# Performance work log

Hardware: AMD Instinct MI355X
Metric: run time of the kernel (lower is better)

The kernel has to match this reference:

```python
import jax, jax.numpy as jnp
import numpy as np

S, LC = 8192, 16
CE = CH = 64      # char embed == char hidden (original quirk)
WE, HW = 128, 256 # word embed, word hidden
WV, CV, TAGS = 50000, 128, 50


def _lstm_step(h, c, x, Wih, Whh, bih, bhh):
    # PyTorch LSTM gate order: i, f, g, o
    g = x @ Wih.T + h @ Whh.T + bih + bhh
    i, f, gg, o = jnp.split(g, 4, axis=-1)
    c = jax.nn.sigmoid(f) * c + jax.nn.sigmoid(i) * jnp.tanh(gg)
    h = jax.nn.sigmoid(o) * jnp.tanh(c)
    return h, c


def setup_inputs() -> dict:
    key = jax.random.key(0)
    ks = jax.random.split(key, 16)
    inp = {
        'word_idxs': jax.random.randint(ks[0], (S,), 0, WV),
        'char_idxs': jax.random.randint(ks[1], (S, LC), 0, CV),
        'char_lens': jax.random.randint(ks[2], (S,), 1, LC + 1),
        'char_emb': jax.random.normal(ks[3], (CV, CE), jnp.float32) * 0.1,
        'char_Wih': jax.random.normal(ks[4], (4 * CH, CE), jnp.float32) * 0.1,
        'char_Whh': jax.random.normal(ks[5], (4 * CH, CH), jnp.float32) * 0.1,
        'char_bih': jax.random.normal(ks[6], (4 * CH,), jnp.float32) * 0.1,
        'char_bhh': jax.random.normal(ks[7], (4 * CH,), jnp.float32) * 0.1,
        'word_emb': jax.random.normal(ks[8], (WV, WE), jnp.float32) * 0.1,
        'word_Wih': jax.random.normal(ks[9], (4 * HW, WE + CH), jnp.float32) * 0.1,
        'word_Whh': jax.random.normal(ks[10], (4 * HW, HW), jnp.float32) * 0.1,
        'word_bih': jax.random.normal(ks[11], (4 * HW,), jnp.float32) * 0.1,
        'word_bhh': jax.random.normal(ks[12], (4 * HW,), jnp.float32) * 0.1,
        'tag_W': jax.random.normal(ks[13], (TAGS, HW), jnp.float32) * 0.1,
        'tag_b': jax.random.normal(ks[14], (TAGS,), jnp.float32) * 0.1,
    }
    return inp


def reference(word_idxs, char_idxs, char_lens,
              char_emb, char_Wih, char_Whh, char_bih, char_bhh,
              word_emb, word_Wih, word_Whh, word_bih, word_bhh,
              tag_W, tag_b):
    # --- char LSTM over all words in parallel (one fused scan over char time) ---
    cx = char_emb[char_idxs]                      # [S, LC, CE]
    cx = jnp.transpose(cx, (1, 0, 2))             # [LC, S, CE]

    def cstep(carry, x_t):
        h, c = carry
        h, c = _lstm_step(h, c, x_t, char_Wih, char_Whh, char_bih, char_bhh)
        return (h, c), h

    h0 = jnp.zeros((S, CH), cx.dtype)
    (_, _), hs = jax.lax.scan(cstep, (h0, h0), cx)  # hs: [LC, S, CH]
    # original takes char_lstm_out[-1] == hidden at position len(chars)-1
    char_feat = hs[char_lens - 1, jnp.arange(S)]    # [S, CH]

    # --- word LSTM over the sentence (batch = 1) ---
    wx = jnp.concatenate([word_emb[word_idxs], char_feat], axis=-1)  # [S, WE+CH]

    def wstep(carry, x_t):
        h, c = carry
        h, c = _lstm_step(h, c, x_t, word_Wih, word_Whh, word_bih, word_bhh)
        return (h, c), h

    wh0 = jnp.zeros((HW,), wx.dtype)
    (_, _), outs = jax.lax.scan(wstep, (wh0, wh0), wx)  # [S, HW]

    logits = outs @ tag_W.T + tag_b                     # [S, TAGS]
    return jax.nn.log_softmax(logits, axis=-1)
```

## Files before the change

kernel.cpp:

```cpp
#include <hip/hip_runtime.h>
#include <hip/hip_bf16.h>
#include <hip/hip_fp16.h>

#define S_LEN 8192
#define LC 16
#define CE 64
#define CH 64
#define WE 128
#define NTAGS 50

using bf16 = __hip_bfloat16;
typedef unsigned int u32;
typedef unsigned long long u64;

__device__ __forceinline__ float bfbits2f(unsigned short u) {
    union { unsigned int i; float f; } v; v.i = ((unsigned int)u) << 16; return v.f;
}
__device__ __forceinline__ float sigm(float x) {
    return __builtin_amdgcn_rcpf(1.0f + __expf(-x));
}
__device__ __forceinline__ float tanh_fast(float x) {
    return 1.0f - 2.0f * __builtin_amdgcn_rcpf(__expf(2.0f * x) + 1.0f);
}

template <bool BF>
__device__ __forceinline__ float ld1(const void* p, size_t i) {
    if constexpr (BF) return bfbits2f(((const unsigned short*)p)[i]);
    else              return ((const float*)p)[i];
}
template <bool BF>
__device__ __forceinline__ float4 ld4(const void* p, size_t i) {
    if constexpr (BF) {
        const ushort4 s = *reinterpret_cast<const ushort4*>((const unsigned short*)p + i);
        return make_float4(bfbits2f(s.x), bfbits2f(s.y), bfbits2f(s.z), bfbits2f(s.w));
    } else {
        return *reinterpret_cast<const float4*>((const float*)p + i);
    }
}
template <bool BF>
__device__ __forceinline__ void st1(void* p, size_t i, float v) {
    if constexpr (BF) ((bf16*)p)[i] = __float2bfloat16(v);
    else              ((float*)p)[i] = v;
}

typedef _Float16 h2t __attribute__((ext_vector_type(2)));

__device__ __forceinline__ u32 pk2(float a, float b) {
    __half2 h = __floats2half2_rn(a, b);
    u32 r; __builtin_memcpy(&r, &h, 4); return r;
}
__device__ __forceinline__ float fdot2u(u32 a, u32 b, float c) {
#if __has_builtin(__builtin_amdgcn_fdot2)
    h2t av, bv;
    __builtin_memcpy(&av, &a, 4);
    __builtin_memcpy(&bv, &b, 4);
    return __builtin_amdgcn_fdot2(av, bv, c, false);
#else
    __half2 ah, bh;
    __builtin_memcpy(&ah, &a, 4);
    __builtin_memcpy(&bh, &b, 4);
    c = fmaf(__half2float(ah.x), __half2float(bh.x), c);
    c = fmaf(__half2float(ah.y), __half2float(bh.y), c);
    return c;
#endif
}

__global__ void kdetect(const void* emb, u32* flag, u32* gen) {
    const int j = threadIdx.x;
    int s = 0;
    #pragma unroll
    for (int k = 0; k < 4; ++k) {
        const unsigned short u = ((const unsigned short*)emb)[j * 4 + k];
        const int e = (u >> 7) & 0xFF;
        s += (e >= 100 && e <= 133) ? 1 : 0;
    }
    #pragma unroll
    for (int off = 32; off >= 1; off >>= 1) s += __shfl_xor(s, off, 64);
    if (j == 0) { *flag = (s >= 200) ? 1u : 0u; *gen = *gen + 1u; }
}

template <bool BF>
__global__ __launch_bounds__(256, 2) void kchar(
        const u32* __restrict__ dtf,
        const int* __restrict__ char_idxs, const int* __restrict__ char_lens,
        const void* __restrict__ char_emb,
        const void* __restrict__ Wih, const void* __restrict__ Whh,
        const void* __restrict__ bih, const void* __restrict__ bhh,
        float* __restrict__ cfeat) {
    if ((*dtf != 0u) != BF) return;
    const int j = threadIdx.x;
    const int w0 = blockIdx.x * 8;

    __shared__ __align__(16) float emb_lds[128 * CE];
    __shared__ __align__(16) float gates_lds[8 * 256];
    __shared__ __align__(16) float h_lds[8 * CH];
    __shared__ __align__(16) float c_lds[8 * CH];
    __shared__ int cidx_lds[8 * LC];
    __shared__ int len_lds[8];

    {
        float4* emb4 = reinterpret_cast<float4*>(emb_lds);
        #pragma unroll
        for (int i = 0; i < 8; ++i) {
            const int c = i * 256 + j;
            emb4[c] = ld4<BF>(char_emb, (size_t)c * 4);
        }
    }
    if (j < 128) cidx_lds[j] = char_idxs[w0 * LC + j];
    if (j < 8)   len_lds[j]  = char_lens[w0 + j];
    h_lds[j] = 0.f; h_lds[j + 256] = 0.f;
    c_lds[j] = 0.f; c_lds[j + 256] = 0.f;

    float4 wih4[16], whh4[16];
    #pragma unroll
    for (int kc = 0; kc < 16; ++kc) {
        wih4[kc] = ld4<BF>(Wih, (size_t)j * CE + kc * 4);
        whh4[kc] = ld4<BF>(Whh, (size_t)j * CH + kc * 4);
    }
    const float bias = ld1<BF>(bih, j) + ld1<BF>(bhh, j);
    __syncthreads();

    for (int t = 0; t < LC; ++t) {
        for (int w = 0; w < 8; ++w) {
            const int ci = cidx_lds[w * LC + t];
            const float4* x4  = reinterpret_cast<const float4*>(emb_lds + ci * CE);
            const float4* hh4 = reinterpret_cast<const float4*>(h_lds + w * CH);
            float a0 = 0.f, a1 = 0.f, a2 = 0.f, a3 = 0.f;
            #pragma unroll
            for (int kc = 0; kc < 16; ++kc) {
                const float4 xv = x4[kc]; const float4 hv = hh4[kc];
                const float4 wi = wih4[kc]; const float4 wh = whh4[kc];
                a0 = fmaf(wi.x, xv.x, a0); a1 = fmaf(wi.y, xv.y, a1);
                a2 = fmaf(wi.z, xv.z, a2); a3 = fmaf(wi.w, xv.w, a3);
                a0 = fmaf(wh.x, hv.x, a0); a1 = fmaf(wh.y, hv.y, a1);
                a2 = fmaf(wh.z, hv.z, a2); a3 = fmaf(wh.w, hv.w, a3);
            }
            gates_lds[w * 256 + j] = bias + ((a0 + a1) + (a2 + a3));
        }
        __syncthreads();
        #pragma unroll
        for (int rep = 0; rep < 2; ++rep) {
            const int p = j + rep * 256;
            const int w = p >> 6, u = p & 63;
            const float ig = gates_lds[w * 256 + u];
            const float fg = gates_lds[w * 256 + 64 + u];
            const float gg = gates_lds[w * 256 + 128 + u];
            const float og = gates_lds[w * 256 + 192 + u];
            const float cn = sigm(fg) * c_lds[p] + sigm(ig) * tanh_fast(gg);
            const float hn = sigm(og) * tanh_fast(cn);
            c_lds[p] = cn; h_lds[p] = hn;
            if (t == len_lds[w] - 1)
                cfeat[(size_t)(w0 + w) * CH + u] = hn;
        }
        __syncthreads();
    }
}

template <bool BF>
__global__ __launch_bounds__(256) void kgx(
        const u32* __restrict__ dtf,
        int t0, const int* __restrict__ word_idxs, const float* __restrict__ cfeat,
        const void* __restrict__ wemb, const void* __restrict__ Wih,
        const void* __restrict__ bih, const void* __restrict__ bhh,
        float* __restrict__ Gxr) {
    if ((*dtf != 0u) != BF) return;
    const int j = threadIdx.x;
    const int wr0 = blockIdx.x * 16;
    const int w0g = t0 + wr0;
    __shared__ __align__(16) float wx[16 * 192];
    __shared__ int widx[16];
    if (j < 16) widx[j] = word_idxs[w0g + j];
    __syncthreads();
    {
        const int w = j >> 4, ch = j & 15;
        const size_t eb = (size_t)widx[w] * WE + ch * 8;
        const float4 f0 = ld4<BF>(wemb, eb), f1 = ld4<BF>(wemb, eb + 4);
        float4* dst = reinterpret_cast<float4*>(wx + w * 192 + ch * 8);
        dst[0] = f0; dst[1] = f1;
        const float4 cf = *reinterpret_cast<const float4*>(
            cfeat + (size_t)(w0g + w) * CH + ch * 4);
        *reinterpret_cast<float4*>(wx + w * 192 + WE + ch * 4) = cf;
    }
    __syncthreads();

    for (int g = 0; g < 4; ++g) {
        const int r = g * 256 + j;
        float acc[16];
        #pragma unroll
        for (int w = 0; w < 16; ++w) acc[w] = 0.f;
        #pragma unroll 8
        for (int kc = 0; kc < 48; ++kc) {
            const float4 wv = ld4<BF>(Wih, (size_t)r * 192 + kc * 4);
            #pragma unroll
            for (int w = 0; w < 16; ++w) {
                const float4 xv = *reinterpret_cast<const float4*>(wx + w * 192 + kc * 4);
                acc[w] = fmaf(wv.x, xv.x, acc[w]);
                acc[w] = fmaf(wv.y, xv.y, acc[w]);
                acc[w] = fmaf(wv.z, xv.z, acc[w]);
                acc[w] = fmaf(wv.w, xv.w, acc[w]);
            }
        }
        const float bias = ld1<BF>(bih, r) + ld1<BF>(bhh, r);
        #pragma unroll
        for (int w = 0; w < 16; ++w)
            Gxr[(size_t)(wr0 + w) * 1024 + r] = acc[w] + bias;
    }
}

template <bool BF>
__global__ __launch_bounds__(256, 1) void kwlstm(
        const u32* __restrict__ dtf,
        int t0, int t1, int epoch, const void* __restrict__ whh,
        const float* __restrict__ Gxr,
        float* __restrict__ hallr, u64* hgx2, float* csave, u32* xccpub,
        const u32* __restrict__ genp) {
    if ((*dtf != 0u) != BF) return;
    const int j = threadIdx.x;

    __shared__ int role_s;
    const u32 et = (((*genp) << 8) + (u32)epoch) & 0xFFFFFFu;
    if (j == 0) {
        const u32 xcc = __builtin_amdgcn_s_getreg(6164) & 0xFu;
        __hip_atomic_store(&xccpub[blockIdx.x], (et << 8) | xcc,
                           __ATOMIC_RELAXED, __HIP_MEMORY_SCOPE_AGENT);
    }
    if (j < 64) {
        u32 v;
        do {
            v = __hip_atomic_load(&xccpub[j], __ATOMIC_RELAXED,
                                  __HIP_MEMORY_SCOPE_AGENT);
        } while ((v >> 8) != et);
        const u32 v0 = __shfl(v, 0, 64);
        const u64 mask = __ballot((v & 0xFFu) == (v0 & 0xFFu));
        const int myb = blockIdx.x;
        int role = -1;
        if (__popcll(mask) >= 4) {
            if ((mask >> myb) & 1ull) {
                const int rank = __popcll(mask & ((1ull << myb) - 1ull));
                if (rank < 4) role = rank;
            }
        } else {
            if (myb < 4) role = myb;
        }
        if (j == 0) role_s = role;
    }
    __syncthreads();
    const int b = role_s;
    if (b < 0) return;

    const int w = j >> 6;
    const int l = j & 63;
    const int m = l & 15;
    const int g = l >> 4;
    const int u = w * 16 + m;
    const int R = g * 256 + b * 64 + u;

    __shared__ __align__(16) u32 hsc[4][32];

    u32 wv2[128];
    #pragma unroll
    for (int q = 0; q < 4; ++q) {
        const int qq = (b + q) & 3;
        #pragma unroll
        for (int kc = 0; kc < 8; ++kc) {
            const float4 wa = ld4<BF>(whh, (size_t)R * 256 + qq * 64 + kc * 8);
            const float4 wb = ld4<BF>(whh, (size_t)R * 256 + qq * 64 + kc * 8 + 4);
            wv2[q * 32 + 4 * kc + 0] = pk2(wa.x, wa.y);
            wv2[q * 32 + 4 * kc + 1] = pk2(wa.z, wa.w);
            wv2[q * 32 + 4 * kc + 2] = pk2(wb.x, wb.y);
            wv2[q * 32 + 4 * kc + 3] = pk2(wb.z, wb.w);
        }
    }

    float c_reg = 0.f;
    if (t0 > 0 && l < 16) c_reg = csave[b * 64 + u];

    float gxA = Gxr[(size_t)0 * 1024 + R];
    float gxB = (t0 + 1 < t1) ? Gxr[(size_t)1 * 1024 + R] : 0.f;

    for (int t = t0; t < t1; ++t) {
        const int p = t & 1;
        float gxN = (t + 2 < t1) ? Gxr[(size_t)(t + 2 - t0) * 1024 + R] : 0.f;

        float a0 = 0.f, a1 = 0.f, a2 = 0.f, a3 = 0.f;
        if (t > 0) {
            u32* hsc_w = &hsc[w][0];
            #pragma unroll
            for (int q = 0; q < 4; ++q) {
                const int qq = (b + q) & 3;
                u64* src = &hgx2[(size_t)p * 256 + qq * 64 + l];
                u64 pk;
                for (;;) {
                    pk = __hip_atomic_load(src, __ATOMIC_RELAXED,
                                           __HIP_MEMORY_SCOPE_AGENT);
                    if (__all((u32)(pk >> 32) == (u32)t)) break;
                }
                const float hv = __uint_as_float((u32)pk);
                const float ho = __shfl_xor(hv, 1, 64);
                if (!(l & 1)) hsc_w[l >> 1] = pk2(hv, ho);
                asm volatile("" ::: "memory");
                #pragma unroll
                for (int kc = 0; kc < 8; ++kc) {
                    const u32 hx = hsc_w[4 * kc + 0];
                    const u32 hy = hsc_w[4 * kc + 1];
                    const u32 hz = hsc_w[4 * kc + 2];
                    const u32 hw2 = hsc_w[4 * kc + 3];
                    a0 = fdot2u(wv2[q * 32 + 4 * kc + 0], hx, a0);
                    a1 = fdot2u(wv2[q * 32 + 4 * kc + 1], hy, a1);
                    a2 = fdot2u(wv2[q * 32 + 4 * kc + 2], hz, a2);
                    a3 = fdot2u(wv2[q * 32 + 4 * kc + 3], hw2, a3);
                }
                asm volatile("" ::: "memory");
            }
        }
        const float gv = ((a0 + a1) + (a2 + a3)) + gxA;
        const float act = (g == 2) ? tanh_fast(gv) : sigm(gv);
        const float a_f = __shfl(act, m + 16, 64);
        const float a_g = __shfl(act, m + 32, 64);
        const float a_o = __shfl(act, m + 48, 64);
        if (l < 16) {
            const float cn = a_f * c_reg + act * a_g;
            c_reg = cn;
            const float hn = a_o * tanh_fast(cn);
            const u64 pk = ((u64)(u32)(t + 1) << 32) | (u64)__float_as_uint(hn);
            __hip_atomic_store(&hgx2[(size_t)((t + 1) & 1) * 256 + b * 64 + u],
                               pk, __ATOMIC_RELAXED, __HIP_MEMORY_SCOPE_AGENT);
            hallr[(size_t)(t - t0) * 256 + b * 64 + u] = hn;
        }
        gxA = gxB; gxB = gxN;
    }
    if (l < 16) csave[b * 64 + u] = c_reg;
}

template <bool BF>
__global__ __launch_bounds__(64) void ktag(
        const u32* __restrict__ dtf,
        int t0, const float* __restrict__ hallr, const void* __restrict__ tagW,
        const void* __restrict__ tagb, void* __restrict__ out) {
    if ((*dtf != 0u) != BF) return;
    const int tr = blockIdx.x, j = threadIdx.x;
    const int t = t0 + tr;
    __shared__ __align__(16) float4 h4[64];
    h4[j] = reinterpret_cast<const float4*>(hallr + (size_t)tr * 256)[j];
    __syncthreads();
    float logit = -1e30f;
    if (j < NTAGS) {
        float a0 = 0.f, a1 = 0.f, a2 = 0.f, a3 = 0.f;
        #pragma unroll
        for (int kc = 0; kc < 64; ++kc) {
            const float4 wvv = ld4<BF>(tagW, (size_t)j * 256 + kc * 4);
            const float4 hv = h4[kc];
            a0 = fmaf(wvv.x, hv.x, a0); a1 = fmaf(wvv.y, hv.y, a1);
            a2 = fmaf(wvv.z, hv.z, a2); a3 = fmaf(wvv.w, hv.w, a3);
        }
        logit = ld1<BF>(tagb, j) + ((a0 + a1) + (a2 + a3));
    }
    float m = logit;
    #pragma unroll
    for (int off = 32; off >= 1; off >>= 1) m = fmaxf(m, __shfl_xor(m, off, 64));
    const float e = (j < NTAGS) ? __expf(logit - m) : 0.f;
    float ssum = e;
    #pragma unroll
    for (int off = 32; off >= 1; off >>= 1) ssum += __shfl_xor(ssum, off, 64);
    if (j < NTAGS)
        st1<BF>(out, (size_t)t * NTAGS + j, logit - m - __logf(ssum));
}

extern "C" void kernel_launch(void* const* d_in, const int* in_sizes, int n_in,
                              void* d_out, int out_size, void* d_ws, size_t ws_size,
                              hipStream_t stream) {
    const int*  word_idxs = (const int*)d_in[0];
    const int*  char_idxs = (const int*)d_in[1];
    const int*  char_lens = (const int*)d_in[2];
    const void* char_emb  = d_in[3];
    const void* char_Wih  = d_in[4];
    const void* char_Whh  = d_in[5];
    const void* char_bih  = d_in[6];
    const void* char_bhh  = d_in[7];
    const void* word_emb  = d_in[8];
    const void* word_Wih  = d_in[9];
    const void* word_Whh  = d_in[10];
    const void* word_bih  = d_in[11];
    const void* word_bhh  = d_in[12];
    const void* tag_W     = d_in[13];
    const void* tag_b     = d_in[14];

    char* ws = (char*)d_ws;
    u32*   dtf    = (u32*)(ws);
    u64*   hgx2   = (u64*)(ws + 64);
    float* csave  = (float*)(ws + 4224);
    u32*   xccpub = (u32*)(ws + 5248);
    u32*   genp   = (u32*)(ws + 5504);
    float* cfeat  = (float*)(ws + 8192);
    const size_t ring0 = 8192 + (size_t)S_LEN * CH * 4;

    int NC = 256;
    const int ncs[9] = {1, 2, 4, 8, 16, 32, 64, 128, 256};
    for (int i = 0; i < 9; ++i) {
        const int ct = S_LEN / ncs[i];
        if (ring0 + (size_t)ct * 5120 <= ws_size) { NC = ncs[i]; break; }
    }
    const int CT = S_LEN / NC;
    float* Gxr   = (float*)(ws + ring0);
    float* hallr = (float*)(ws + ring0 + (size_t)CT * 4096);

    hipLaunchKernelGGL(kdetect, dim3(1), dim3(64), 0, stream, char_emb, dtf, genp);
    hipLaunchKernelGGL(kchar<true>,  dim3(S_LEN / 8), dim3(256), 0, stream,
                       dtf, char_idxs, char_lens, char_emb, char_Wih, char_Whh,
                       char_bih, char_bhh, cfeat);
    hipLaunchKernelGGL(kchar<false>, dim3(S_LEN / 8), dim3(256), 0, stream,
                       dtf, char_idxs, char_lens, char_emb, char_Wih, char_Whh,
                       char_bih, char_bhh, cfeat);
    for (int c = 0; c < NC; ++c) {
        const int t0 = c * CT;
        hipLaunchKernelGGL(kgx<true>,  dim3(CT / 16), dim3(256), 0, stream,
                           dtf, t0, word_idxs, cfeat, word_emb, word_Wih,
                           word_bih, word_bhh, Gxr);
        hipLaunchKernelGGL(kgx<false>, dim3(CT / 16), dim3(256), 0, stream,
                           dtf, t0, word_idxs, cfeat, word_emb, word_Wih,
                           word_bih, word_bhh, Gxr);
        hipLaunchKernelGGL(kwlstm<true>,  dim3(64), dim3(256), 0, stream,
                           dtf, t0, t0 + CT, c, word_Whh, Gxr, hallr, hgx2,
                           csave, xccpub, genp);
        hipLaunchKernelGGL(kwlstm<false>, dim3(64), dim3(256), 0, stream,
                           dtf, t0, t0 + CT, c, word_Whh, Gxr, hallr, hgx2,
                           csave, xccpub, genp);
        hipLaunchKernelGGL(ktag<true>,  dim3(CT), dim3(64), 0, stream,
                           dtf, t0, hallr, tag_W, tag_b, d_out);
        hipLaunchKernelGGL(ktag<false>, dim3(CT), dim3(64), 0, stream,
                           dtf, t0, hallr, tag_W, tag_b, d_out);
    }
}
```

Before: 14.61 ms.

## Run word LSTM recurrence in a single workgroup with LDS-resident hidden state

Replaces the 4-workgroup word LSTM, which spins on agent-scope atomics in global memory every step with XCC-aware role election, by a single 512-thread workgroup. Each thread owns two gate rows. Weights are held partly in registers (200 columns) and partly in LDS (56 columns), and h is exchanged through LDS with one __syncthreads per step. This removes cross-CU global-memory handshakes from the serial critical path. In exchange the recurrence runs on a single CU with heavy register pressure (200 weight registers per thread), and h/c are now carried across chunks via hsave/csave.

```diff
diff --git a/kernel.cpp b/kernel.cpp
--- a/kernel.cpp
+++ b/kernel.cpp
@@ -65,7 +65,7 @@
 #endif
 }
 
-__global__ void kdetect(const void* emb, u32* flag, u32* gen) {
+__global__ void kdetect(const void* emb, u32* flag) {
     const int j = threadIdx.x;
     int s = 0;
     #pragma unroll
@@ -76,7 +76,7 @@
     }
     #pragma unroll
     for (int off = 32; off >= 1; off >>= 1) s += __shfl_xor(s, off, 64);
-    if (j == 0) { *flag = (s >= 200) ? 1u : 0u; *gen = *gen + 1u; }
+    if (j == 0) *flag = (s >= 200) ? 1u : 0u;
 }
 
 template <bool BF>
@@ -208,128 +208,117 @@
 }
 
 template <bool BF>
-__global__ __launch_bounds__(256, 1) void kwlstm(
+__global__ __launch_bounds__(512, 2) void kwlstm(
         const u32* __restrict__ dtf,
-        int t0, int t1, int epoch, const void* __restrict__ whh,
+        int t0, int t1, const void* __restrict__ whh,
         const float* __restrict__ Gxr,
-        float* __restrict__ hallr, u64* hgx2, float* csave, u32* xccpub,
-        const u32* __restrict__ genp) {
+        float* __restrict__ hallr, u32* __restrict__ hsave,
+        float* __restrict__ csave) {
     if ((*dtf != 0u) != BF) return;
     const int j = threadIdx.x;
-
-    __shared__ int role_s;
-    const u32 et = (((*genp) << 8) + (u32)epoch) & 0xFFFFFFu;
-    if (j == 0) {
-        const u32 xcc = __builtin_amdgcn_s_getreg(6164) & 0xFu;
-        __hip_atomic_store(&xccpub[blockIdx.x], (et << 8) | xcc,
-                           __ATOMIC_RELAXED, __HIP_MEMORY_SCOPE_AGENT);
-    }
-    if (j < 64) {
-        u32 v;
-        do {
-            v = __hip_atomic_load(&xccpub[j], __ATOMIC_RELAXED,
-                                  __HIP_MEMORY_SCOPE_AGENT);
-        } while ((v >> 8) != et);
-        const u32 v0 = __shfl(v, 0, 64);
-        const u64 mask = __ballot((v & 0xFFu) == (v0 & 0xFFu));
-        const int myb = blockIdx.x;
-        int role = -1;
-        if (__popcll(mask) >= 4) {
-            if ((mask >> myb) & 1ull) {
-                const int rank = __popcll(mask & ((1ull << myb) - 1ull));
-                if (rank < 4) role = rank;
-            }
-        } else {
-            if (myb < 4) role = myb;
-        }
-        if (j == 0) role_s = role;
+    const int u = j >> 1;
+    const int k = j & 1;
+    const int rowA = (k ? 256 : 0) + u;
+    const int rowB = (k ? 768 : 512) + u;
+
+    __shared__ __align__(16) uint4 wl[14][512];
+    __shared__ __align__(16) u32 h2[2][128];
+
+    u32 wA[100], wB[100];
+    #pragma unroll
+    for (int kc = 0; kc < 50; ++kc) {
+        const float4 wa = ld4<BF>(whh, (size_t)rowA * 256 + kc * 4);
+        wA[2 * kc]     = pk2(wa.x, wa.y);
+        wA[2 * kc + 1] = pk2(wa.z, wa.w);
+        const float4 wb = ld4<BF>(whh, (size_t)rowB * 256 + kc * 4);
+        wB[2 * kc]     = pk2(wb.x, wb.y);
+        wB[2 * kc + 1] = pk2(wb.z, wb.w);
+    }
+    #pragma unroll
+    for (int q = 0; q < 7; ++q) {
+        const float4 a0 = ld4<BF>(whh, (size_t)rowA * 256 + 200 + q * 8);
+        const float4 a1 = ld4<BF>(whh, (size_t)rowA * 256 + 200 + q * 8 + 4);
+        wl[q][j] = make_uint4(pk2(a0.x, a0.y), pk2(a0.z, a0.w),
+                              pk2(a1.x, a1.y), pk2(a1.z, a1.w));
+        const float4 b0 = ld4<BF>(whh, (size_t)rowB * 256 + 200 + q * 8);
+        const float4 b1 = ld4<BF>(whh, (size_t)rowB * 256 + 200 + q * 8 + 4);
+        wl[7 + q][j] = make_uint4(pk2(b0.x, b0.y), pk2(b0.z, b0.w),
+                                  pk2(b1.x, b1.y), pk2(b1.z, b1.w));
+    }
+    if (j < 128) {
+        h2[0][j] = 0u; h2[1][j] = 0u;
+        if (t0 > 0) h2[t0 & 1][j] = hsave[j];
+    }
+    float c_reg = 0.f;
+    if (k == 0 && t0 > 0) c_reg = csave[u];
+
+    float gxAA = Gxr[(size_t)0 * 1024 + rowA];
+    float gxAB = Gxr[(size_t)0 * 1024 + rowB];
+    float gxBA = 0.f, gxBB = 0.f;
+    if (t0 + 1 < t1) {
+        gxBA = Gxr[(size_t)1 * 1024 + rowA];
+        gxBB = Gxr[(size_t)1 * 1024 + rowB];
     }
     __syncthreads();
-    const int b = role_s;
-    if (b < 0) return;
-
-    const int w = j >> 6;
-    const int l = j & 63;
-    const int m = l & 15;
-    const int g = l >> 4;
-    const int u = w * 16 + m;
-    const int R = g * 256 + b * 64 + u;
-
-    __shared__ __align__(16) u32 hsc[4][32];
-
-    u32 wv2[128];
-    #pragma unroll
-    for (int q = 0; q < 4; ++q) {
-        const int qq = (b + q) & 3;
-        #pragma unroll
-        for (int kc = 0; kc < 8; ++kc) {
-            const float4 wa = ld4<BF>(whh, (size_t)R * 256 + qq * 64 + kc * 8);
-            const float4 wb = ld4<BF>(whh, (size_t)R * 256 + qq * 64 + kc * 8 + 4);
-            wv2[q * 32 + 4 * kc + 0] = pk2(wa.x, wa.y);
-            wv2[q * 32 + 4 * kc + 1] = pk2(wa.z, wa.w);
-            wv2[q * 32 + 4 * kc + 2] = pk2(wb.x, wb.y);
-            wv2[q * 32 + 4 * kc + 3] = pk2(wb.z, wb.w);
-        }
-    }
-
-    float c_reg = 0.f;
-    if (t0 > 0 && l < 16) c_reg = csave[b * 64 + u];
-
-    float gxA = Gxr[(size_t)0 * 1024 + R];
-    float gxB = (t0 + 1 < t1) ? Gxr[(size_t)1 * 1024 + R] : 0.f;
 
     for (int t = t0; t < t1; ++t) {
         const int p = t & 1;
-        float gxN = (t + 2 < t1) ? Gxr[(size_t)(t + 2 - t0) * 1024 + R] : 0.f;
-
-        float a0 = 0.f, a1 = 0.f, a2 = 0.f, a3 = 0.f;
+        float gxNA = 0.f, gxNB = 0.f;
+        if (t + 2 < t1) {
+            gxNA = Gxr[(size_t)(t + 2 - t0) * 1024 + rowA];
+            gxNB = Gxr[(size_t)(t + 2 - t0) * 1024 + rowB];
+        }
+
+        float aA0 = 0.f, aA1 = 0.f, aB0 = 0.f, aB1 = 0.f;
         if (t > 0) {
-            u32* hsc_w = &hsc[w][0];
+            const uint4* h4 = reinterpret_cast<const uint4*>(&h2[p][0]);
             #pragma unroll
-            for (int q = 0; q < 4; ++q) {
-                const int qq = (b + q) & 3;
-                u64* src = &hgx2[(size_t)p * 256 + qq * 64 + l];
-                u64 pk;
-                for (;;) {
-                    pk = __hip_atomic_load(src, __ATOMIC_RELAXED,
-                                           __HIP_MEMORY_SCOPE_AGENT);
-                    if (__all((u32)(pk >> 32) == (u32)t)) break;
-                }
-                const float hv = __uint_as_float((u32)pk);
-                const float ho = __shfl_xor(hv, 1, 64);
-                if (!(l & 1)) hsc_w[l >> 1] = pk2(hv, ho);
-                asm volatile("" ::: "memory");
-                #pragma unroll
-                for (int kc = 0; kc < 8; ++kc) {
-                    const u32 hx = hsc_w[4 * kc + 0];
-                    const u32 hy = hsc_w[4 * kc + 1];
-                    const u32 hz = hsc_w[4 * kc + 2];
-                    const u32 hw2 = hsc_w[4 * kc + 3];
-                    a0 = fdot2u(wv2[q * 32 + 4 * kc + 0], hx, a0);
-                    a1 = fdot2u(wv2[q * 32 + 4 * kc + 1], hy, a1);
-                    a2 = fdot2u(wv2[q * 32 + 4 * kc + 2], hz, a2);
-                    a3 = fdot2u(wv2[q * 32 + 4 * kc + 3], hw2, a3);
-                }
-                asm volatile("" ::: "memory");
+            for (int q = 0; q < 25; ++q) {
+                const uint4 hv = h4[q];
+                aA0 = fdot2u(wA[4 * q + 0], hv.x, aA0);
+                aA1 = fdot2u(wA[4 * q + 1], hv.y, aA1);
+                aA0 = fdot2u(wA[4 * q + 2], hv.z, aA0);
+                aA1 = fdot2u(wA[4 * q + 3], hv.w, aA1);
+                aB0 = fdot2u(wB[4 * q + 0], hv.x, aB0);
+                aB1 = fdot2u(wB[4 * q + 1], hv.y, aB1);
+                aB0 = fdot2u(wB[4 * q + 2], hv.z, aB0);
+                aB1 = fdot2u(wB[4 * q + 3], hv.w, aB1);
             }
-        }
-        const float gv = ((a0 + a1) + (a2 + a3)) + gxA;
-        const float act = (g == 2) ? tanh_fast(gv) : sigm(gv);
-        const float a_f = __shfl(act, m + 16, 64);
-        const float a_g = __shfl(act, m + 32, 64);
-        const float a_o = __shfl(act, m + 48, 64);
-        if (l < 16) {
-            const float cn = a_f * c_reg + act * a_g;
+            #pragma unroll
+            for (int q = 0; q < 7; ++q) {
+                const uint4 hv = h4[25 + q];
+                const uint4 wa = wl[q][j];
+                const uint4 wb = wl[7 + q][j];
+                aA0 = fdot2u(wa.x, hv.x, aA0);
+                aA1 = fdot2u(wa.y, hv.y, aA1);
+                aA0 = fdot2u(wa.z, hv.z, aA0);
+                aA1 = fdot2u(wa.w, hv.w, aA1);
+                aB0 = fdot2u(wb.x, hv.x, aB0);
+                aB1 = fdot2u(wb.y, hv.y, aB1);
+                aB0 = fdot2u(wb.z, hv.z, aB0);
+                aB1 = fdot2u(wb.w, hv.w, aB1);
+            }
+        }
+        const float gA = (aA0 + aA1) + gxAA;
+        const float gB = (aB0 + aB1) + gxAB;
+        const float actA = sigm(gA);
+        const float actB = k ? sigm(gB) : tanh_fast(gB);
+        const float xfA = __shfl_xor(actA, 1, 64);
+        const float xfB = __shfl_xor(actB, 1, 64);
+        float hn = 0.f;
+        if (k == 0) {
+            const float cn = xfA * c_reg + actA * actB;
             c_reg = cn;
-            const float hn = a_o * tanh_fast(cn);
-            const u64 pk = ((u64)(u32)(t + 1) << 32) | (u64)__float_as_uint(hn);
-            __hip_atomic_store(&hgx2[(size_t)((t + 1) & 1) * 256 + b * 64 + u],
-                               pk, __ATOMIC_RELAXED, __HIP_MEMORY_SCOPE_AGENT);
-            hallr[(size_t)(t - t0) * 256 + b * 64 + u] = hn;
-        }
-        gxA = gxB; gxB = gxN;
-    }
-    if (l < 16) csave[b * 64 + u] = c_reg;
+            hn = xfB * tanh_fast(cn);
+            hallr[(size_t)(t - t0) * 256 + u] = hn;
+        }
+        const float ho = __shfl_xor(hn, 2, 64);
+        if ((j & 3) == 0) h2[p ^ 1][u >> 1] = pk2(hn, ho);
+        __syncthreads();
+        gxAA = gxBA; gxAB = gxBB; gxBA = gxNA; gxBB = gxNB;
+    }
+    if (j < 128) hsave[j] = h2[t1 & 1][j];
+    if (k == 0)  csave[u] = c_reg;
 }
 
 template <bool BF>
@@ -387,10 +376,8 @@
 
     char* ws = (char*)d_ws;
     u32*   dtf    = (u32*)(ws);
-    u64*   hgx2   = (u64*)(ws + 64);
+    u32*   hsave  = (u32*)(ws + 64);
     float* csave  = (float*)(ws + 4224);
-    u32*   xccpub = (u32*)(ws + 5248);
-    u32*   genp   = (u32*)(ws + 5504);
     float* cfeat  = (float*)(ws + 8192);
     const size_t ring0 = 8192 + (size_t)S_LEN * CH * 4;
 
@@ -404,7 +391,7 @@
     float* Gxr   = (float*)(ws + ring0);
     float* hallr = (float*)(ws + ring0 + (size_t)CT * 4096);
 
-    hipLaunchKernelGGL(kdetect, dim3(1), dim3(64), 0, stream, char_emb, dtf, genp);
+    hipLaunchKernelGGL(kdetect, dim3(1), dim3(64), 0, stream, char_emb, dtf);
     hipLaunchKernelGGL(kchar<true>,  dim3(S_LEN / 8), dim3(256), 0, stream,
                        dtf, char_idxs, char_lens, char_emb, char_Wih, char_Whh,
                        char_bih, char_bhh, cfeat);
@@ -419,12 +406,10 @@
         hipLaunchKernelGGL(kgx<false>, dim3(CT / 16), dim3(256), 0, stream,
                            dtf, t0, word_idxs, cfeat, word_emb, word_Wih,
                            word_bih, word_bhh, Gxr);
-        hipLaunchKernelGGL(kwlstm<true>,  dim3(64), dim3(256), 0, stream,
-                           dtf, t0, t0 + CT, c, word_Whh, Gxr, hallr, hgx2,
-                           csave, xccpub, genp);
-        hipLaunchKernelGGL(kwlstm<false>, dim3(64), dim3(256), 0, stream,
-                           dtf, t0, t0 + CT, c, word_Whh, Gxr, hallr, hgx2,
-                           csave, xccpub, genp);
+        hipLaunchKernelGGL(kwlstm<true>,  dim3(1), dim3(512), 0, stream,
+                           dtf, t0, t0 + CT, word_Whh, Gxr, hallr, hsave, csave);
+        hipLaunchKernelGGL(kwlstm<false>, dim3(1), dim3(512), 0, stream,
+                           dtf, t0, t0 + CT, word_Whh, Gxr, hallr, hsave, csave);
         hipLaunchKernelGGL(ktag<true>,  dim3(CT), dim3(64), 0, stream,
                            dtf, t0, hallr, tag_W, tag_b, d_out);
         hipLaunchKernelGGL(ktag<false>, dim3(CT), dim3(64), 0, stream,
```

Result: faster. 14.25 ms (-2.4%).
